# Kernel optimization log

Measured on AMD Instinct MI355X. Metric: run time of the kernel, lower is better.

## Reference

```python
import jax, jax.numpy as jnp
import numpy as np

N_NODES = 50000
N_GRAPHS = 4
N_EDGES = 800000
D_IN = 128
D_OUT = 128


def setup_inputs() -> dict:
    key = jax.random.key(0)
    ks = jax.random.split(key, 7)
    x = jax.random.normal(ks[0], (N_NODES, D_IN), dtype=jnp.float32)
    edge_rows = jax.random.randint(ks[1], (N_GRAPHS, N_EDGES), 0, N_NODES, dtype=jnp.int32)
    edge_cols = jax.random.randint(ks[2], (N_GRAPHS, N_EDGES), 0, N_NODES, dtype=jnp.int32)
    edge_vals = jax.random.uniform(ks[3], (N_GRAPHS, N_EDGES), dtype=jnp.float32)
    W = jax.random.normal(ks[4], (N_GRAPHS, D_IN, D_OUT), dtype=jnp.float32) * (1.0 / np.sqrt(D_IN))
    mixing_weight = jax.random.uniform(ks[5], (N_GRAPHS, 1), dtype=jnp.float32, minval=-0.25, maxval=0.25)
    bias = jax.random.uniform(ks[6], (D_OUT,), dtype=jnp.float32, minval=-0.25, maxval=0.25)
    return {"x": x, "edge_rows": edge_rows, "edge_cols": edge_cols,
            "edge_vals": edge_vals, "W": W, "mixing_weight": mixing_weight, "bias": bias}


def _spmm(rows, cols, vals, dense):
    # sparse [N,N] (COO) @ dense [N,F] -> [N,F]
    gathered = dense[cols] * vals[:, None]          # [E, F]
    return jax.ops.segment_sum(gathered, rows, num_segments=N_NODES)


def reference(x, edge_rows, edge_cols, edge_vals, W, mixing_weight, bias):
    # Per-graph linear projection: [L, N, F_out]
    pre_sup = jnp.einsum('nd,ldf->lnf', x, W)
    # Per-graph spmm via vmap over graphs
    graph_outputs = jax.vmap(_spmm)(edge_rows, edge_cols, edge_vals, pre_sup)  # [L, N, F_out]
    # Weighted mix across graphs (tensordot + squeeze in torch)
    out = jnp.einsum('l,lnf->nf', mixing_weight[:, 0], graph_outputs)
    return out + bias
```

## Files before the change

### kernel.cpp

```cpp
#include <hip/hip_runtime.h>


constexpr int N = 50000;
constexpr int E = 800000;
constexpr int D = 128;
constexpr int L = 4;
constexpr int BSH = 4;
constexpr int NB = N >> BSH;
constexpr int NCHK = 100;
constexpr int CHUNK = E / NCHK;
constexpr int CAP = 1024;

typedef __attribute__((ext_vector_type(8))) short bf16x8;
typedef __attribute__((ext_vector_type(4))) float f32x4;
union U4B8 { uint4 u; bf16x8 b; };

__device__ inline unsigned bf16rne(unsigned u) {
    return (u + 0x7FFFu + ((u >> 16) & 1u)) >> 16;
}

__global__ __launch_bounds__(256) void cvt_x_kernel(
    const float* __restrict__ x, unsigned* __restrict__ xb)
{
    int i = blockIdx.x * 256 + threadIdx.x;
    int row = i >> 6, j = i & 63;
    int q = j >> 4, fl = j & 15;
    float2 v = *reinterpret_cast<const float2*>(x + (size_t)row * D + q * 32 + fl * 2);
    xb[((size_t)q * N + row) * 16 + fl] =
        bf16rne(__float_as_uint(v.x)) | (bf16rne(__float_as_uint(v.y)) << 16);
}

__global__ __launch_bounds__(256) void cvt_w_kernel(
    const float* __restrict__ W, const float* __restrict__ mix,
    unsigned* __restrict__ WbT)
{
    int idx = blockIdx.x * 256 + threadIdx.x;
    int f = idx & 127, dp = (idx >> 7) & 63, l = idx >> 13;
    float m = mix[l];
    float a = m * W[((size_t)l * D + 2 * dp) * D + f];
    float b = m * W[((size_t)l * D + 2 * dp + 1) * D + f];
    WbT[((size_t)l * D + f) * 64 + dp] =
        bf16rne(__float_as_uint(a)) | (bf16rne(__float_as_uint(b)) << 16);
}

__global__ __launch_bounds__(256) void hist_kernel(
    const int* __restrict__ edge_rows,
    unsigned short* __restrict__ pcnt,
    unsigned short* __restrict__ chunkoff)
{
    __shared__ int cnt[NB];
    __shared__ int psum[256];
    const int blk = blockIdx.x, g = blockIdx.y, tid = threadIdx.x;

    for (int i = tid; i < NB; i += 256) cnt[i] = 0;
    __syncthreads();

    const int* rows = edge_rows + (size_t)g * E + (size_t)blk * CHUNK;
    for (int i = tid; i < CHUNK; i += 256)
        atomicAdd(&cnt[rows[i] >> BSH], 1);
    __syncthreads();

    unsigned short* pc = pcnt + ((size_t)g * NCHK + blk) * NB;
    for (int i = tid; i < NB; i += 256) pc[i] = (unsigned short)cnt[i];
    __syncthreads();

    constexpr int CB = (NB + 255) / 256;
    const int base = tid * CB;
    int s = 0;
#pragma unroll
    for (int j = 0; j < CB; ++j) {
        int idx = base + j;
        if (idx < NB) s += cnt[idx];
    }
    psum[tid] = s;
    __syncthreads();
    for (int off = 1; off < 256; off <<= 1) {
        int v = (tid >= off) ? psum[tid - off] : 0;
        __syncthreads();
        psum[tid] += v;
        __syncthreads();
    }
    int carry = (tid == 0) ? 0 : psum[tid - 1];
#pragma unroll
    for (int j = 0; j < CB; ++j) {
        int idx = base + j;
        if (idx < NB) {
            int c = cnt[idx];
            cnt[idx] = carry;
            carry += c;
        }
    }
    __syncthreads();

    unsigned short* co = chunkoff + ((size_t)g * NCHK + blk) * NB;
    for (int i = tid; i < NB; i += 256) co[i] = (unsigned short)cnt[i];
}

__global__ __launch_bounds__(256) void scatter_kernel(
    const int* __restrict__ edge_rows,
    const int* __restrict__ edge_cols,
    const float* __restrict__ edge_vals,
    const unsigned short* __restrict__ chunkoff,
    unsigned* __restrict__ cvT,
    unsigned char* __restrict__ rlT)
{
    __shared__ unsigned cur[(NB + 1) / 2];
    __shared__ unsigned lcv[CHUNK];
    __shared__ unsigned char lrl[CHUNK];
    const int blk = blockIdx.x, g = blockIdx.y, tid = threadIdx.x;

    const unsigned short* co = chunkoff + ((size_t)g * NCHK + blk) * NB;
    for (int i = tid; i < (NB + 1) / 2; i += 256) {
        unsigned lo = co[2 * i];
        unsigned hi = (2 * i + 1 < NB) ? co[2 * i + 1] : 0u;
        cur[i] = lo | (hi << 16);
    }
    __syncthreads();

    const size_t eoff = (size_t)g * E + (size_t)blk * CHUNK;
    const int* rows = edge_rows + eoff;
    const int* cols = edge_cols + eoff;
    const float* vals = edge_vals + eoff;

    for (int i = tid; i < CHUNK; i += 256) {
        int r = rows[i];
        int b = r >> BSH;
        unsigned old = atomicAdd(&cur[b >> 1], (b & 1) ? 0x10000u : 1u);
        int pos = (old >> ((b & 1) * 16)) & 0xFFFFu;
        lcv[pos] = (unsigned)cols[i] | (bf16rne(__float_as_uint(vals[i])) << 16);
        lrl[pos] = (unsigned char)(r & 15);
    }
    __syncthreads();

    unsigned* cw = cvT + eoff;
    unsigned char* rw = rlT + eoff;
    for (int i = tid; i < CHUNK; i += 256) cw[i] = lcv[i];
    for (int i = tid * 4; i < CHUNK; i += 1024)
        *reinterpret_cast<uint*>(rw + i) = *reinterpret_cast<const uint*>(lrl + i);
}

__global__ __launch_bounds__(256) void scan1_kernel(
    unsigned short* __restrict__ pcnt, int* __restrict__ bstart)
{
    const int b = blockIdx.x * 256 + threadIdx.x;
    const int g = blockIdx.y;
    if (b >= NB) return;
    unsigned run = 0;
    unsigned short* p = pcnt + (size_t)g * NCHK * NB + b;
    for (int blk = 0; blk < NCHK; ++blk) {
        unsigned v = p[(size_t)blk * NB];
        p[(size_t)blk * NB] = (unsigned short)run;
        run += v;
    }
    bstart[(size_t)g * (NB + 1) + b] = (int)run;
}

__global__ __launch_bounds__(1024) void scan2_kernel(int* __restrict__ bstart)
{
    __shared__ int sums[1024];
    int* bs = bstart + (size_t)blockIdx.x * (NB + 1);
    const int t = threadIdx.x;
    int tv[4];
    int s = 0;
#pragma unroll
    for (int i = 0; i < 4; ++i) {
        int idx = t * 4 + i;
        tv[i] = (idx < NB) ? bs[idx] : 0;
        s += tv[i];
    }
    sums[t] = s;
    __syncthreads();
    for (int off = 1; off < 1024; off <<= 1) {
        int v = (t >= off) ? sums[t - off] : 0;
        __syncthreads();
        sums[t] += v;
        __syncthreads();
    }
    int ex = (t == 0) ? 0 : sums[t - 1];
#pragma unroll
    for (int i = 0; i < 4; ++i) {
        int idx = t * 4 + i;
        if (idx < NB) { bs[idx] = ex; ex += tv[i]; }
    }
    if (t == 0) bs[NB] = E;
}

__global__ __launch_bounds__(256) void sort2_kernel(
    const unsigned* __restrict__ cvT,
    const unsigned char* __restrict__ rlT,
    const unsigned short* __restrict__ pcnt,
    const unsigned short* __restrict__ chunkoff,
    const int* __restrict__ bstart,
    unsigned* __restrict__ cv,
    int* __restrict__ rowptr)
{
    __shared__ unsigned su_cv[CAP], ss_cv[CAP];
    __shared__ unsigned char su_rl[CAP];
    __shared__ int rc[17], rcur[16];
    const int b = blockIdx.x, g = blockIdx.y, tid = threadIdx.x;
    const int beg = bstart[(size_t)g * (NB + 1) + b];
    const int tot = bstart[(size_t)g * (NB + 1) + b + 1] - beg;
    const int cnt = tot < CAP ? tot : CAP;
    int* rp = rowptr + (size_t)g * (N + 1);
    if (b == 0 && tid == 0) rp[N] = E;
    if (tid < 17) rc[tid] = 0;

    if (tid < NCHK) {
        const int c = tid;
        const size_t pbase = ((size_t)g * NCHK + c) * NB + b;
        int off = pcnt[pbase];
        int nxt = (c == NCHK - 1) ? tot : (int)pcnt[pbase + NB];
        int len = nxt - off;
        const size_t wbase = (size_t)g * E + (size_t)c * CHUNK + chunkoff[pbase];
        const unsigned* cw = cvT + wbase;
        const unsigned char* rw = rlT + wbase;
        for (int i = 0; i < len; ++i) {
            int p = off + i;
            if (p < CAP) { su_cv[p] = cw[i]; su_rl[p] = rw[i]; }
        }
    }
    __syncthreads();

    for (int i = tid; i < cnt; i += 256) atomicAdd(&rc[su_rl[i] + 1], 1);
    __syncthreads();
    if (tid == 0) {
        int run = 0;
#pragma unroll
        for (int r = 1; r <= 16; ++r) { run += rc[r]; rc[r] = run; }
    }
    __syncthreads();
    if (tid < 16) {
        rcur[tid] = rc[tid];
        rp[b * 16 + tid] = beg + rc[tid];
    }
    __syncthreads();
    for (int i = tid; i < cnt; i += 256) {
        int p = atomicAdd(&rcur[su_rl[i]], 1);
        ss_cv[p] = su_cv[i];
    }
    __syncthreads();
    unsigned* cvg = cv + (size_t)g * E;
    for (int i = tid; i < cnt; i += 256) cvg[beg + i] = ss_cv[i];
}

__global__ __launch_bounds__(256) void fused_kernel(
    const unsigned* __restrict__ xb,
    const unsigned* __restrict__ cv,
    const int* __restrict__ rowptr,
    const unsigned* __restrict__ WbT,
    const float* __restrict__ bias,
    float* __restrict__ out,
    int q)
{
    __shared__ unsigned tile[2][16][16];

    const int tid = threadIdx.x;
    const int lane = tid & 63;
    const int wave = tid >> 6;
    const int sub = lane >> 4;
    const int fl = lane & 15;
    const int subbase = lane & 48;
    const int trow = wave * 4 + sub;
    const int row = blockIdx.x * 16 + trow;
    const int lrow = lane & 15, kgrp = lane >> 4;

    const unsigned* xq = xb + (size_t)q * N * 16;

    f32x4 acc[2] = {};
    int tb = 0;

    for (int l = 0; l < L; ++l) {
        const unsigned* cvg = cv + (size_t)l * E;
        const int* rp = rowptr + (size_t)l * (N + 1);
        const int beg = rp[row], end = rp[row + 1];
        float accx = 0.f, accy = 0.f;

        for (int base = beg; base < end; base += 16) {
            const int cnt = end - base;
            unsigned cvr = (fl < cnt) ? cvg[base + fl] : 0u;
            const int ng = cnt < 13 ? ((cnt + 3) >> 2) : 4;
            for (int kg = 0; kg < ng; ++kg) {
                const int kb = subbase + kg * 4;
                unsigned c0 = __shfl(cvr, kb + 0);
                unsigned c1 = __shfl(cvr, kb + 1);
                unsigned c2 = __shfl(cvr, kb + 2);
                unsigned c3 = __shfl(cvr, kb + 3);
                unsigned x0 = xq[(size_t)(c0 & 0xFFFFu) * 16 + fl];
                unsigned x1 = xq[(size_t)(c1 & 0xFFFFu) * 16 + fl];
                unsigned x2 = xq[(size_t)(c2 & 0xFFFFu) * 16 + fl];
                unsigned x3 = xq[(size_t)(c3 & 0xFFFFu) * 16 + fl];
                float v0 = __uint_as_float(c0 & 0xFFFF0000u);
                float v1 = __uint_as_float(c1 & 0xFFFF0000u);
                float v2 = __uint_as_float(c2 & 0xFFFF0000u);
                float v3 = __uint_as_float(c3 & 0xFFFF0000u);
                accx = fmaf(v0, __uint_as_float(x0 << 16), accx);
                accy = fmaf(v0, __uint_as_float(x0 & 0xFFFF0000u), accy);
                accx = fmaf(v1, __uint_as_float(x1 << 16), accx);
                accy = fmaf(v1, __uint_as_float(x1 & 0xFFFF0000u), accy);
                accx = fmaf(v2, __uint_as_float(x2 << 16), accx);
                accy = fmaf(v2, __uint_as_float(x2 & 0xFFFF0000u), accy);
                accx = fmaf(v3, __uint_as_float(x3 << 16), accx);
                accy = fmaf(v3, __uint_as_float(x3 & 0xFFFF0000u), accy);
            }
        }
        tile[tb][trow][fl] = bf16rne(__float_as_uint(accx)) |
                             (bf16rne(__float_as_uint(accy)) << 16);
        __syncthreads();

        U4B8 a;
        a.u = *reinterpret_cast<const uint4*>(&tile[tb][lrow][kgrp * 4]);
#pragma unroll
        for (int t = 0; t < 2; ++t) {
            const int f = wave * 32 + t * 16 + lrow;
            U4B8 bb;
            bb.u = *reinterpret_cast<const uint4*>(
                WbT + ((size_t)l * D + f) * 64 + q * 16 + kgrp * 4);
            acc[t] = __builtin_amdgcn_mfma_f32_16x16x32_bf16(a.b, bb.b, acc[t], 0, 0, 0);
        }
        tb ^= 1;
    }

#pragma unroll
    for (int t = 0; t < 2; ++t) {
        const int f = wave * 32 + t * 16 + lrow;
#pragma unroll
        for (int i = 0; i < 4; ++i) {
            int orow = blockIdx.x * 16 + kgrp * 4 + i;
            float* p = out + (size_t)orow * D + f;
            float v = acc[t][i];
            *p = (q == 0) ? v + bias[f] : *p + v;
        }
    }
}

extern "C" void kernel_launch(void* const* d_in, const int* in_sizes, int n_in,
                              void* d_out, int out_size, void* d_ws, size_t ws_size,
                              hipStream_t stream)
{
    const float* x         = (const float*)d_in[0];
    const int*   edge_rows = (const int*)d_in[1];
    const int*   edge_cols = (const int*)d_in[2];
    const float* edge_vals = (const float*)d_in[3];
    const float* W         = (const float*)d_in[4];
    const float* mix       = (const float*)d_in[5];
    const float* bias      = (const float*)d_in[6];
    float* out = (float*)d_out;

    unsigned*       cvT      = (unsigned*)d_ws;
    unsigned char*  rlT      = (unsigned char*)(cvT + (size_t)L * E);
    unsigned short* pcnt     = (unsigned short*)(rlT + (size_t)L * E);
    unsigned short* chunkoff = pcnt + (size_t)L * NCHK * NB;
    int*            bstart   = (int*)(chunkoff + (size_t)L * NCHK * NB);
    int*            rowptr   = bstart + (size_t)L * (NB + 1);
    unsigned*       cv       = (unsigned*)(rowptr + (size_t)L * (N + 1));
    unsigned*       xb       = cv + (size_t)L * E;
    unsigned*       WbT      = xb + (size_t)4 * N * 16;

    cvt_x_kernel<<<(N * 64) / 256, 256, 0, stream>>>(x, xb);
    cvt_w_kernel<<<(L * D * 64) / 256, 256, 0, stream>>>(W, mix, WbT);
    hist_kernel<<<dim3(NCHK, L), 256, 0, stream>>>(edge_rows, pcnt, chunkoff);
    scatter_kernel<<<dim3(NCHK, L), 256, 0, stream>>>(edge_rows, edge_cols,
                                                      edge_vals, chunkoff, cvT, rlT);
    scan1_kernel<<<dim3((NB + 255) / 256, L), 256, 0, stream>>>(pcnt, bstart);
    scan2_kernel<<<L, 1024, 0, stream>>>(bstart);
    sort2_kernel<<<dim3(NB, L), 256, 0, stream>>>(cvT, rlT, pcnt, chunkoff, bstart,
                                                  cv, rowptr);

    for (int q = 0; q < 4; ++q)
        fused_kernel<<<N / 16, 256, 0, stream>>>(xb, cv, rowptr, WbT, bias, out, q);
}
```

Measured before the change: 301.6 us.

## Assign one graph per wave and reduce graph outputs through LDS atomics

Each of the four waves in a block now handles one graph's SpMM over all 16 rows of the block, instead of every wave looping over all four graphs. This removes the block-wide barrier between graphs. Each wave runs its own MFMA projection over all 128 output columns, and the results from the four graphs are summed with shared-memory float atomics before one coalesced write to global memory. The inner gather loop is now fully unrolled with no early exit, so short rows do extra, harmless loads of row 0 in exchange for less control flow. The shared-memory accumulator and atomics add LDS traffic and occupancy pressure.

After: 815.8 us. +170.5%, slower.

```diff
diff --git a/kernel.cpp b/kernel.cpp
--- a/kernel.cpp
+++ b/kernel.cpp
@@ -252,7 +252,8 @@
     float* __restrict__ out,
     int q)
 {
-    __shared__ unsigned tile[2][16][16];
+    __shared__ unsigned tile[4][16][16];
+    __shared__ float accL[16][D];
 
     const int tid = threadIdx.x;
     const int lane = tid & 63;
@@ -260,27 +261,27 @@
     const int sub = lane >> 4;
     const int fl = lane & 15;
     const int subbase = lane & 48;
-    const int trow = wave * 4 + sub;
-    const int row = blockIdx.x * 16 + trow;
+    const int b = blockIdx.x;
     const int lrow = lane & 15, kgrp = lane >> 4;
 
+    for (int i = tid; i < 16 * D; i += 256) ((float*)accL)[i] = 0.f;
+    __syncthreads();
+
     const unsigned* xq = xb + (size_t)q * N * 16;
-
-    f32x4 acc[2] = {};
-    int tb = 0;
-
-    for (int l = 0; l < L; ++l) {
-        const unsigned* cvg = cv + (size_t)l * E;
-        const int* rp = rowptr + (size_t)l * (N + 1);
+    const unsigned* cvg = cv + (size_t)wave * E;
+    const int* rp = rowptr + (size_t)wave * (N + 1);
+
+    for (int j = 0; j < 4; ++j) {
+        const int trow = sub * 4 + j;
+        const int row = b * 16 + trow;
         const int beg = rp[row], end = rp[row + 1];
         float accx = 0.f, accy = 0.f;
-
         for (int base = beg; base < end; base += 16) {
             const int cnt = end - base;
             unsigned cvr = (fl < cnt) ? cvg[base + fl] : 0u;
-            const int ng = cnt < 13 ? ((cnt + 3) >> 2) : 4;
-            for (int kg = 0; kg < ng; ++kg) {
-                const int kb = subbase + kg * 4;
+#pragma unroll
+            for (int k = 0; k < 16; k += 4) {
+                const int kb = subbase + k;
                 unsigned c0 = __shfl(cvr, kb + 0);
                 unsigned c1 = __shfl(cvr, kb + 1);
                 unsigned c2 = __shfl(cvr, kb + 2);
@@ -303,33 +304,35 @@
                 accy = fmaf(v3, __uint_as_float(x3 & 0xFFFF0000u), accy);
             }
         }
-        tile[tb][trow][fl] = bf16rne(__float_as_uint(accx)) |
-                             (bf16rne(__float_as_uint(accy)) << 16);
-        __syncthreads();
-
-        U4B8 a;
-        a.u = *reinterpret_cast<const uint4*>(&tile[tb][lrow][kgrp * 4]);
-#pragma unroll
-        for (int t = 0; t < 2; ++t) {
-            const int f = wave * 32 + t * 16 + lrow;
-            U4B8 bb;
-            bb.u = *reinterpret_cast<const uint4*>(
-                WbT + ((size_t)l * D + f) * 64 + q * 16 + kgrp * 4);
-            acc[t] = __builtin_amdgcn_mfma_f32_16x16x32_bf16(a.b, bb.b, acc[t], 0, 0, 0);
-        }
-        tb ^= 1;
-    }
-
-#pragma unroll
-    for (int t = 0; t < 2; ++t) {
-        const int f = wave * 32 + t * 16 + lrow;
-#pragma unroll
-        for (int i = 0; i < 4; ++i) {
-            int orow = blockIdx.x * 16 + kgrp * 4 + i;
-            float* p = out + (size_t)orow * D + f;
-            float v = acc[t][i];
-            *p = (q == 0) ? v + bias[f] : *p + v;
-        }
+        tile[wave][trow][fl] = bf16rne(__float_as_uint(accx)) |
+                               (bf16rne(__float_as_uint(accy)) << 16);
+    }
+    asm volatile("s_waitcnt lgkmcnt(0)" ::: "memory");
+
+    U4B8 a;
+    a.u = *reinterpret_cast<const uint4*>(&tile[wave][lrow][kgrp * 4]);
+    f32x4 acc[8];
+#pragma unroll
+    for (int t = 0; t < 8; ++t) {
+        const int f = t * 16 + lrow;
+        U4B8 bb;
+        bb.u = *reinterpret_cast<const uint4*>(
+            WbT + ((size_t)wave * D + f) * 64 + q * 16 + kgrp * 4);
+        f32x4 z = {};
+        acc[t] = __builtin_amdgcn_mfma_f32_16x16x32_bf16(a.b, bb.b, z, 0, 0, 0);
+    }
+#pragma unroll
+    for (int t = 0; t < 8; ++t)
+#pragma unroll
+        for (int i = 0; i < 4; ++i)
+            atomicAdd(&accL[kgrp * 4 + i][t * 16 + lrow], acc[t][i]);
+    __syncthreads();
+
+    for (int i = tid; i < 16 * D; i += 256) {
+        int r = i >> 7, f = i & 127;
+        float v = accL[r][f];
+        float* p = out + (size_t)(b * 16 + r) * D + f;
+        *p = (q == 0) ? v + bias[f] : *p + v;
     }
 }
 
@@ -367,5 +370,5 @@
                                                   cv, rowptr);
 
     for (int q = 0; q < 4; ++q)
-        fused_kernel<<<N / 16, 256, 0, stream>>>(xb, cv, rowptr, WbT, bias, out, q);
-}
+        fused_kernel<<<NB, 256, 0, stream>>>(xb, cv, rowptr, WbT, bias, out, q);
+}
```

## Partition SpMM passes by column range instead of feature quarter

Applied to the files above, without the earlier changes.

Instead of splitting the four fused passes by feature quarter, edges are sorted within each row by column range, so each pass gathers full 128-feature rows from one quarter of the node table, which should fit better in cache. The sort kernel now keys on (column group, row) and emits per-block 17-entry segment pointers for each column group. The fused kernel loads 16 bytes per lane per neighbour and runs four MFMA k-chunks per graph. The cost is more MFMA work and more W reads per pass, a larger shared tile, and more complex row pointers.

Result: slower. 396.5 us (+31.5%).

```diff
diff --git a/kernel.cpp b/kernel.cpp
--- a/kernel.cpp
+++ b/kernel.cpp
@@ -7,6 +7,7 @@
 constexpr int L = 4;
 constexpr int BSH = 4;
 constexpr int NB = N >> BSH;
+constexpr int NBINS = NB * 4;
 constexpr int NCHK = 100;
 constexpr int CHUNK = E / NCHK;
 constexpr int CAP = 1024;
@@ -18,16 +19,17 @@
 __device__ inline unsigned bf16rne(unsigned u) {
     return (u + 0x7FFFu + ((u >> 16) & 1u)) >> 16;
 }
+__device__ inline int cgof(int col) {
+    return (col >= 25000) ? ((col >= 37500) ? 3 : 2)
+                          : ((col >= 12500) ? 1 : 0);
+}
 
 __global__ __launch_bounds__(256) void cvt_x_kernel(
     const float* __restrict__ x, unsigned* __restrict__ xb)
 {
     int i = blockIdx.x * 256 + threadIdx.x;
-    int row = i >> 6, j = i & 63;
-    int q = j >> 4, fl = j & 15;
-    float2 v = *reinterpret_cast<const float2*>(x + (size_t)row * D + q * 32 + fl * 2);
-    xb[((size_t)q * N + row) * 16 + fl] =
-        bf16rne(__float_as_uint(v.x)) | (bf16rne(__float_as_uint(v.y)) << 16);
+    float2 v = reinterpret_cast<const float2*>(x)[i];
+    xb[i] = bf16rne(__float_as_uint(v.x)) | (bf16rne(__float_as_uint(v.y)) << 16);
 }
 
 __global__ __launch_bounds__(256) void cvt_w_kernel(
@@ -192,18 +194,16 @@
     const unsigned short* __restrict__ chunkoff,
     const int* __restrict__ bstart,
     unsigned* __restrict__ cv,
-    int* __restrict__ rowptr)
+    int* __restrict__ rp17)
 {
     __shared__ unsigned su_cv[CAP], ss_cv[CAP];
-    __shared__ unsigned char su_rl[CAP];
-    __shared__ int rc[17], rcur[16];
+    __shared__ unsigned char su_k[CAP];
+    __shared__ int rc[65], rcur[64];
     const int b = blockIdx.x, g = blockIdx.y, tid = threadIdx.x;
     const int beg = bstart[(size_t)g * (NB + 1) + b];
     const int tot = bstart[(size_t)g * (NB + 1) + b + 1] - beg;
     const int cnt = tot < CAP ? tot : CAP;
-    int* rp = rowptr + (size_t)g * (N + 1);
-    if (b == 0 && tid == 0) rp[N] = E;
-    if (tid < 17) rc[tid] = 0;
+    if (tid < 65) rc[tid] = 0;
 
     if (tid < NCHK) {
         const int c = tid;
@@ -216,43 +216,48 @@
         const unsigned char* rw = rlT + wbase;
         for (int i = 0; i < len; ++i) {
             int p = off + i;
-            if (p < CAP) { su_cv[p] = cw[i]; su_rl[p] = rw[i]; }
-        }
-    }
-    __syncthreads();
-
-    for (int i = tid; i < cnt; i += 256) atomicAdd(&rc[su_rl[i] + 1], 1);
+            if (p < CAP) { su_cv[p] = cw[i]; su_k[p] = rw[i]; }
+        }
+    }
+    __syncthreads();
+
+    for (int i = tid; i < cnt; i += 256) {
+        int key = cgof((int)(su_cv[i] & 0xFFFFu)) * 16 + (int)su_k[i];
+        su_k[i] = (unsigned char)key;
+        atomicAdd(&rc[key + 1], 1);
+    }
     __syncthreads();
     if (tid == 0) {
         int run = 0;
 #pragma unroll
-        for (int r = 1; r <= 16; ++r) { run += rc[r]; rc[r] = run; }
-    }
-    __syncthreads();
-    if (tid < 16) {
-        rcur[tid] = rc[tid];
-        rp[b * 16 + tid] = beg + rc[tid];
-    }
+        for (int r = 1; r <= 64; ++r) { run += rc[r]; rc[r] = run; }
+    }
+    __syncthreads();
+    if (tid < 64) rcur[tid] = rc[tid];
     __syncthreads();
     for (int i = tid; i < cnt; i += 256) {
-        int p = atomicAdd(&rcur[su_rl[i]], 1);
+        int p = atomicAdd(&rcur[su_k[i]], 1);
         ss_cv[p] = su_cv[i];
     }
     __syncthreads();
     unsigned* cvg = cv + (size_t)g * E;
     for (int i = tid; i < cnt; i += 256) cvg[beg + i] = ss_cv[i];
+    if (tid < 68) {
+        int cgi = tid / 17, t = tid % 17;
+        rp17[((size_t)g * NBINS + b * 4 + cgi) * 17 + t] = beg + rc[cgi * 16 + t];
+    }
 }
 
 __global__ __launch_bounds__(256) void fused_kernel(
     const unsigned* __restrict__ xb,
     const unsigned* __restrict__ cv,
-    const int* __restrict__ rowptr,
+    const int* __restrict__ rp17,
     const unsigned* __restrict__ WbT,
     const float* __restrict__ bias,
     float* __restrict__ out,
-    int q)
-{
-    __shared__ unsigned tile[2][16][16];
+    int cg)
+{
+    __shared__ unsigned tile[2][16][68];
 
     const int tid = threadIdx.x;
     const int lane = tid & 63;
@@ -261,61 +266,64 @@
     const int fl = lane & 15;
     const int subbase = lane & 48;
     const int trow = wave * 4 + sub;
-    const int row = blockIdx.x * 16 + trow;
+    const int b = blockIdx.x;
     const int lrow = lane & 15, kgrp = lane >> 4;
-
-    const unsigned* xq = xb + (size_t)q * N * 16;
 
     f32x4 acc[2] = {};
     int tb = 0;
 
     for (int l = 0; l < L; ++l) {
         const unsigned* cvg = cv + (size_t)l * E;
-        const int* rp = rowptr + (size_t)l * (N + 1);
-        const int beg = rp[row], end = rp[row + 1];
-        float accx = 0.f, accy = 0.f;
-
-        for (int base = beg; base < end; base += 16) {
-            const int cnt = end - base;
-            unsigned cvr = (fl < cnt) ? cvg[base + fl] : 0u;
-            const int ng = cnt < 13 ? ((cnt + 3) >> 2) : 4;
+        const int* seg = rp17 + ((size_t)l * NBINS + b * 4 + cg) * 17;
+        const int s0 = seg[trow], s1 = seg[trow + 1];
+
+        float2 a01 = {0.f, 0.f}, a23 = {0.f, 0.f};
+        float2 a45 = {0.f, 0.f}, a67 = {0.f, 0.f};
+
+        for (int base = s0; base < s1; base += 8) {
+            const int cnt = s1 - base;
+            unsigned cvr = (fl < cnt && fl < 8) ? cvg[base + fl] : 0u;
+            const int ng = (cnt >= 8) ? 2 : ((cnt + 3) >> 2);
             for (int kg = 0; kg < ng; ++kg) {
                 const int kb = subbase + kg * 4;
-                unsigned c0 = __shfl(cvr, kb + 0);
-                unsigned c1 = __shfl(cvr, kb + 1);
-                unsigned c2 = __shfl(cvr, kb + 2);
-                unsigned c3 = __shfl(cvr, kb + 3);
-                unsigned x0 = xq[(size_t)(c0 & 0xFFFFu) * 16 + fl];
-                unsigned x1 = xq[(size_t)(c1 & 0xFFFFu) * 16 + fl];
-                unsigned x2 = xq[(size_t)(c2 & 0xFFFFu) * 16 + fl];
-                unsigned x3 = xq[(size_t)(c3 & 0xFFFFu) * 16 + fl];
-                float v0 = __uint_as_float(c0 & 0xFFFF0000u);
-                float v1 = __uint_as_float(c1 & 0xFFFF0000u);
-                float v2 = __uint_as_float(c2 & 0xFFFF0000u);
-                float v3 = __uint_as_float(c3 & 0xFFFF0000u);
-                accx = fmaf(v0, __uint_as_float(x0 << 16), accx);
-                accy = fmaf(v0, __uint_as_float(x0 & 0xFFFF0000u), accy);
-                accx = fmaf(v1, __uint_as_float(x1 << 16), accx);
-                accy = fmaf(v1, __uint_as_float(x1 & 0xFFFF0000u), accy);
-                accx = fmaf(v2, __uint_as_float(x2 << 16), accx);
-                accy = fmaf(v2, __uint_as_float(x2 & 0xFFFF0000u), accy);
-                accx = fmaf(v3, __uint_as_float(x3 << 16), accx);
-                accy = fmaf(v3, __uint_as_float(x3 & 0xFFFF0000u), accy);
+#pragma unroll
+                for (int j = 0; j < 4; ++j) {
+                    unsigned c = __shfl(cvr, kb + j);
+                    float v = __uint_as_float(c & 0xFFFF0000u);
+                    unsigned col = c & 0xFFFFu;
+                    uint4 xv = *reinterpret_cast<const uint4*>(
+                        xb + (size_t)col * 64 + fl * 4);
+                    a01.x = fmaf(v, __uint_as_float(xv.x << 16), a01.x);
+                    a01.y = fmaf(v, __uint_as_float(xv.x & 0xFFFF0000u), a01.y);
+                    a23.x = fmaf(v, __uint_as_float(xv.y << 16), a23.x);
+                    a23.y = fmaf(v, __uint_as_float(xv.y & 0xFFFF0000u), a23.y);
+                    a45.x = fmaf(v, __uint_as_float(xv.z << 16), a45.x);
+                    a45.y = fmaf(v, __uint_as_float(xv.z & 0xFFFF0000u), a45.y);
+                    a67.x = fmaf(v, __uint_as_float(xv.w << 16), a67.x);
+                    a67.y = fmaf(v, __uint_as_float(xv.w & 0xFFFF0000u), a67.y);
+                }
             }
         }
-        tile[tb][trow][fl] = bf16rne(__float_as_uint(accx)) |
-                             (bf16rne(__float_as_uint(accy)) << 16);
-        __syncthreads();
-
-        U4B8 a;
-        a.u = *reinterpret_cast<const uint4*>(&tile[tb][lrow][kgrp * 4]);
-#pragma unroll
-        for (int t = 0; t < 2; ++t) {
-            const int f = wave * 32 + t * 16 + lrow;
-            U4B8 bb;
-            bb.u = *reinterpret_cast<const uint4*>(
-                WbT + ((size_t)l * D + f) * 64 + q * 16 + kgrp * 4);
-            acc[t] = __builtin_amdgcn_mfma_f32_16x16x32_bf16(a.b, bb.b, acc[t], 0, 0, 0);
+        unsigned* tw = &tile[tb][trow][fl * 4];
+        tw[0] = bf16rne(__float_as_uint(a01.x)) | (bf16rne(__float_as_uint(a01.y)) << 16);
+        tw[1] = bf16rne(__float_as_uint(a23.x)) | (bf16rne(__float_as_uint(a23.y)) << 16);
+        tw[2] = bf16rne(__float_as_uint(a45.x)) | (bf16rne(__float_as_uint(a45.y)) << 16);
+        tw[3] = bf16rne(__float_as_uint(a67.x)) | (bf16rne(__float_as_uint(a67.y)) << 16);
+        __syncthreads();
+
+#pragma unroll
+        for (int kc = 0; kc < 4; ++kc) {
+            U4B8 a;
+            a.u = *reinterpret_cast<const uint4*>(&tile[tb][lrow][kc * 16 + kgrp * 4]);
+#pragma unroll
+            for (int t = 0; t < 2; ++t) {
+                const int f = wave * 32 + t * 16 + lrow;
+                U4B8 bb;
+                bb.u = *reinterpret_cast<const uint4*>(
+                    WbT + ((size_t)l * D + f) * 64 + kc * 16 + kgrp * 4);
+                acc[t] = __builtin_amdgcn_mfma_f32_16x16x32_bf16(
+                    a.b, bb.b, acc[t], 0, 0, 0);
+            }
         }
         tb ^= 1;
     }
@@ -325,10 +333,10 @@
         const int f = wave * 32 + t * 16 + lrow;
 #pragma unroll
         for (int i = 0; i < 4; ++i) {
-            int orow = blockIdx.x * 16 + kgrp * 4 + i;
+            int orow = b * 16 + kgrp * 4 + i;
             float* p = out + (size_t)orow * D + f;
             float v = acc[t][i];
-            *p = (q == 0) ? v + bias[f] : *p + v;
+            *p = (cg == 0) ? v + bias[f] : *p + v;
         }
     }
 }
@@ -351,10 +359,10 @@
     unsigned short* pcnt     = (unsigned short*)(rlT + (size_t)L * E);
     unsigned short* chunkoff = pcnt + (size_t)L * NCHK * NB;
     int*            bstart   = (int*)(chunkoff + (size_t)L * NCHK * NB);
-    int*            rowptr   = bstart + (size_t)L * (NB + 1);
-    unsigned*       cv       = (unsigned*)(rowptr + (size_t)L * (N + 1));
+    int*            rp17     = bstart + (size_t)L * (NB + 1);
+    unsigned*       cv       = (unsigned*)(rp17 + (size_t)L * NBINS * 17);
     unsigned*       xb       = cv + (size_t)L * E;
-    unsigned*       WbT      = xb + (size_t)4 * N * 16;
+    unsigned*       WbT      = xb + (size_t)N * 64;
 
     cvt_x_kernel<<<(N * 64) / 256, 256, 0, stream>>>(x, xb);
     cvt_w_kernel<<<(L * D * 64) / 256, 256, 0, stream>>>(W, mix, WbT);
@@ -364,8 +372,8 @@
     scan1_kernel<<<dim3((NB + 255) / 256, L), 256, 0, stream>>>(pcnt, bstart);
     scan2_kernel<<<L, 1024, 0, stream>>>(bstart);
     sort2_kernel<<<dim3(NB, L), 256, 0, stream>>>(cvT, rlT, pcnt, chunkoff, bstart,
-                                                  cv, rowptr);
-
-    for (int q = 0; q < 4; ++q)
-        fused_kernel<<<N / 16, 256, 0, stream>>>(xb, cv, rowptr, WbT, bias, out, q);
-}
+                                                  cv, rp17);
+
+    for (int cg = 0; cg < 4; ++cg)
+        fused_kernel<<<NB, 256, 0, stream>>>(xb, cv, rp17, WbT, bias, out, cg);
+}
```
